# Kernel tuning notes

Hardware: AMD Instinct MI355X
Metric: run time of the kernel (lower is better)

Reference implementation:

```python
import jax, jax.numpy as jnp
import numpy as np

B, V, MAX_TOPK = 256, 128000, 256
IGNORED = -3000.0

def setup_inputs() -> dict:
    key = jax.random.key(0)
    k1, k2, k3, k4, k5 = jax.random.split(key, 5)
    token_logits = jax.random.normal(k1, (B, V), dtype=jnp.float32)
    # sampling_params[:,0]=top_k in [1,256], [:,1]=top_p in [0.5,1.0], [:,2]=temperature in [0.7,1.3]
    top_k = jax.random.randint(k2, (B,), 1, MAX_TOPK + 1).astype(jnp.float32)
    top_p = jax.random.uniform(k3, (B,), minval=0.5, maxval=1.0, dtype=jnp.float32)
    temp = jax.random.uniform(k4, (B,), minval=0.7, maxval=1.3, dtype=jnp.float32)
    sampling_params = jnp.stack([top_k, top_p, temp], axis=1)
    rand_u = jax.random.uniform(k5, (B, 1), dtype=jnp.float32)
    return {"token_logits": token_logits, "sampling_params": sampling_params, "rand_u": rand_u}

def reference(token_logits, sampling_params, rand_u):
    top_k = sampling_params[:, 0:1]        # [B,1] float
    top_p = sampling_params[:, 1:2]        # [B,1]
    temperature = sampling_params[:, 2:3]  # [B,1]
    # top_k candidates over full vocab (max_topk optimization path)
    vals, idx = jax.lax.top_k(token_logits, MAX_TOPK)  # [B,K], [B,K]
    # per-row top_k mask: positions >= top_k get IGNORED
    pos = jnp.arange(MAX_TOPK, dtype=jnp.float32)[None, :]
    vals = jnp.where(pos >= top_k, IGNORED, vals)
    # temperature
    vals = vals / temperature
    probs = jax.nn.softmax(vals, axis=-1)
    csum = jnp.cumsum(probs, axis=-1)
    # top_p clamped by global min of cumsum (matches torch.max(torch.min(csum), top_p))
    top_p_eff = jnp.maximum(jnp.min(csum), top_p)
    pmask = (csum > top_p_eff).at[:, 0].set(False)
    vals = jnp.where(pmask, IGNORED, vals)
    probs = jax.nn.softmax(vals, axis=-1)
    # multinomial via cumsum + rand-compare-sum
    csum2 = jnp.cumsum(probs, axis=-1)
    counts = jnp.sum((rand_u > csum2).astype(jnp.int32), axis=-1)  # [B]
    tokens = jnp.take_along_axis(idx, counts[:, None], axis=-1).reshape(-1)  # [B]
    return tokens
```

## Files before the change

### kernel.cpp

```cpp
#include <hip/hip_runtime.h>
#include <hip/hip_bf16.h>

constexpr int BATCH = 256;
constexpr int VOCAB = 128000;
constexpr int K = 256;
constexpr float IGNORED_C = -3000.0f;

constexpr int NCHUNK = 8;
constexpr int CHUNK = VOCAB / NCHUNK;
constexpr int N4 = CHUNK / 4;
constexpr int BINS = 8192;
constexpr int SHIFT = 19;
constexpr int CAP = 512;

constexpr int FB_BINS = 8192;
constexpr int FB_SHIFT = 19;
constexpr int FB_CAND = 2048;

__device__ __forceinline__ unsigned mono(unsigned u) {
    return (u & 0x80000000u) ? ~u : (u | 0x80000000u);
}
__device__ __forceinline__ float inv_mono(unsigned k) {
    unsigned u = (k & 0x80000000u) ? (k ^ 0x80000000u) : ~k;
    return __uint_as_float(u);
}

__global__ __launch_bounds__(512)
void k1_topk_chunk(const float* __restrict__ logits,
                   unsigned long long* __restrict__ ws_cand)
{
    __shared__ unsigned hist[BINS];
    __shared__ unsigned part[512];
    __shared__ unsigned long long cand[CAP];
    __shared__ unsigned ccount;
    __shared__ int s_tbin;

    const int tid = threadIdx.x;
    const int row = blockIdx.x >> 3;
    const int chunk = blockIdx.x & 7;
    const int gbase = chunk * CHUNK;
    const float4* rp4 = reinterpret_cast<const float4*>(
        logits + (size_t)row * VOCAB + (size_t)gbase);

    for (int i = tid; i < BINS; i += 512) hist[i] = 0u;
    if (tid == 0) ccount = 0u;
    __syncthreads();

    for (int i = tid; i < N4; i += 1024) {
        const float4 va = rp4[i];
        const bool hb = (i + 512) < N4;
        float4 vb;
        if (hb) vb = rp4[i + 512];
        atomicAdd(&hist[mono(__float_as_uint(va.x)) >> SHIFT], 1u);
        atomicAdd(&hist[mono(__float_as_uint(va.y)) >> SHIFT], 1u);
        atomicAdd(&hist[mono(__float_as_uint(va.z)) >> SHIFT], 1u);
        atomicAdd(&hist[mono(__float_as_uint(va.w)) >> SHIFT], 1u);
        if (hb) {
            atomicAdd(&hist[mono(__float_as_uint(vb.x)) >> SHIFT], 1u);
            atomicAdd(&hist[mono(__float_as_uint(vb.y)) >> SHIFT], 1u);
            atomicAdd(&hist[mono(__float_as_uint(vb.z)) >> SHIFT], 1u);
            atomicAdd(&hist[mono(__float_as_uint(vb.w)) >> SHIFT], 1u);
        }
    }
    __syncthreads();

    {
        unsigned s = 0;
        #pragma unroll
        for (int j = 0; j < 16; ++j)
            s += hist[tid * 16 + ((j + tid) & 15)];
        part[tid] = s;
    }
    __syncthreads();

    if (tid < 64) {
        const int l = tid;
        const unsigned g0 = part[l * 8 + 0], g1 = part[l * 8 + 1];
        const unsigned g2 = part[l * 8 + 2], g3 = part[l * 8 + 3];
        const unsigned g4 = part[l * 8 + 4], g5 = part[l * 8 + 5];
        const unsigned g6 = part[l * 8 + 6], g7 = part[l * 8 + 7];
        const unsigned s7 = g7;
        const unsigned s6 = s7 + g6;
        const unsigned s5 = s6 + g5;
        const unsigned s4 = s5 + g4;
        const unsigned s3 = s4 + g3;
        const unsigned s2 = s3 + g2;
        const unsigned s1 = s2 + g1;
        const unsigned s0 = s1 + g0;
        unsigned suf = s0;
        #pragma unroll
        for (int off = 1; off < 64; off <<= 1) {
            unsigned t = __shfl_down(suf, off);
            if (l + off < 64) suf += t;
        }
        const unsigned hi = suf - s0;
        const bool finder = (hi < (unsigned)K) && (hi + s0 >= (unsigned)K);
        int jj; unsigned base;
        if      (hi + s7 >= (unsigned)K) { jj = 7; base = hi; }
        else if (hi + s6 >= (unsigned)K) { jj = 6; base = hi + s7; }
        else if (hi + s5 >= (unsigned)K) { jj = 5; base = hi + s6; }
        else if (hi + s4 >= (unsigned)K) { jj = 4; base = hi + s5; }
        else if (hi + s3 >= (unsigned)K) { jj = 3; base = hi + s4; }
        else if (hi + s2 >= (unsigned)K) { jj = 2; base = hi + s3; }
        else if (hi + s1 >= (unsigned)K) { jj = 1; base = hi + s2; }
        else                             { jj = 0; base = hi + s1; }
        int tg = l * 8 + jj;
        const unsigned long long fm = __ballot(finder);
        const int src = __ffsll((unsigned long long)fm) - 1;
        tg   = __shfl(tg, src);
        base = __shfl(base, src);
        unsigned h = (l < 16) ? hist[tg * 16 + l] : 0u;
        unsigned suf16 = h;
        #pragma unroll
        for (int off = 1; off < 16; off <<= 1) {
            unsigned t = __shfl_down(suf16, off);
            if (l + off < 16) suf16 += t;
        }
        const bool qual = (l < 16) && (base + suf16 >= (unsigned)K);
        const unsigned long long qm = __ballot(qual);
        if (l == 0) s_tbin = tg * 16 + (63 - __builtin_clzll(qm));
    }
    __syncthreads();

    const unsigned tb = (unsigned)s_tbin;
#define COLV(vv, off4) { \
    const unsigned k_ = mono(__float_as_uint(vv)); \
    if ((k_ >> SHIFT) >= tb) { \
        const unsigned p_ = atomicAdd(&ccount, 1u); \
        if (p_ < (unsigned)CAP) \
            cand[p_] = ((unsigned long long)k_ << 32) | (unsigned)(~(off4)); \
    } }
    for (int i = tid; i < N4; i += 1024) {
        const float4 va = rp4[i];
        const bool hb = (i + 512) < N4;
        float4 vb;
        if (hb) vb = rp4[i + 512];
        const int ba = gbase + i * 4;
        COLV(va.x, ba + 0) COLV(va.y, ba + 1) COLV(va.z, ba + 2) COLV(va.w, ba + 3)
        if (hb) {
            const int bb = gbase + (i + 512) * 4;
            COLV(vb.x, bb + 0) COLV(vb.y, bb + 1) COLV(vb.z, bb + 2) COLV(vb.w, bb + 3)
        }
    }
#undef COLV
    __syncthreads();
    const unsigned cc = ccount;
    if ((unsigned)tid >= cc) cand[tid] = 0ull;
    __syncthreads();

    unsigned long long v = cand[tid];
    #pragma unroll
    for (int kk = 2; kk <= CAP; kk <<= 1) {
        for (int j = kk >> 1; j > 0; j >>= 1) {
            const bool keepMax = (((tid & kk) == 0) == ((tid & j) == 0));
            unsigned long long w;
            if (j >= 64) {
                __syncthreads();
                cand[tid] = v;
                __syncthreads();
                w = cand[tid ^ j];
            } else {
                w = __shfl_xor(v, j);
            }
            v = keepMax ? (v >= w ? v : w) : (v <= w ? v : w);
        }
    }

    if (tid < K) ws_cand[(size_t)blockIdx.x * K + tid] = v;
}

__global__ __launch_bounds__(1024)
void k2_merge(const float* __restrict__ params,
              const unsigned long long* __restrict__ ws_cand,
              float* __restrict__ ws_v, float* __restrict__ ws_csum,
              int* __restrict__ ws_idx, float* __restrict__ ws_p0)
{
    constexpr int N = NCHUNK * K;
    __shared__ unsigned long long cand[N];
    __shared__ float red[K];
    __shared__ float sc[K];

    const int row = blockIdx.x;
    const int tid = threadIdx.x;

    for (int i = tid; i < N; i += 1024) {
        const int c = i >> 8, pos = i & (K - 1);
        unsigned long long v = ws_cand[(size_t)row * N + i];
        const int dest = (c & 1) ? ((c << 8) | (K - 1 - pos)) : i;
        cand[dest] = v;
    }
    __syncthreads();

    for (int kk2 = 2 * K; kk2 <= N; kk2 <<= 1) {
        for (int j = kk2 >> 1; j > 0; j >>= 1) {
            for (int i = tid; i < N; i += 1024) {
                const int ixj = i ^ j;
                if (ixj > i) {
                    unsigned long long a = cand[i], b = cand[ixj];
                    bool sw = ((i & kk2) == 0) ? (a < b) : (a > b);
                    if (sw) { cand[i] = b; cand[ixj] = a; }
                }
            }
            __syncthreads();
        }
    }

    const bool act = tid < K;
    const float topk_f = params[row * 3 + 0];
    const float temp   = params[row * 3 + 2];
    float v = 0.f;
    int myidx = 0;
    if (act) {
        unsigned long long c = cand[tid];
        float val = inv_mono((unsigned)(c >> 32));
        myidx = (int)(~(unsigned)c);
        float x = (((float)tid) >= topk_f) ? IGNORED_C : val;
        v = x / temp;
        red[tid] = v;
    }
    __syncthreads();
    for (int s = K / 2; s > 0; s >>= 1) {
        if (tid < s) red[tid] = fmaxf(red[tid], red[tid + s]);
        __syncthreads();
    }
    const float m = red[0];
    __syncthreads();
    const float e = act ? expf(v - m) : 0.f;
    if (act) red[tid] = e;
    __syncthreads();
    for (int s = K / 2; s > 0; s >>= 1) {
        if (tid < s) red[tid] += red[tid + s];
        __syncthreads();
    }
    const float ssum = red[0];
    __syncthreads();
    const float p = e / ssum;
    if (act) sc[tid] = p;
    __syncthreads();
    for (int off = 1; off < K; off <<= 1) {
        float t = 0.f;
        if (act && tid >= off) t = sc[tid - off];
        __syncthreads();
        if (act) sc[tid] += t;
        __syncthreads();
    }
    if (act) {
        ws_v[row * K + tid]    = v;
        ws_csum[row * K + tid] = sc[tid];
        ws_idx[row * K + tid]  = myidx;
    }
    if (tid == 0) ws_p0[row] = p;
}

__global__ __launch_bounds__(K)
void k3_sample(const float* __restrict__ params,
               const float* __restrict__ rand_u,
               const float* __restrict__ ws_v,
               const float* __restrict__ ws_csum,
               const int* __restrict__ ws_idx,
               const float* __restrict__ ws_p0,
               int* __restrict__ out)
{
    __shared__ float red[K];
    __shared__ float sc[K];
    const int row = blockIdx.x;
    const int tid = threadIdx.x;

    red[tid] = ws_p0[tid];
    __syncthreads();
    for (int s = K / 2; s > 0; s >>= 1) {
        if (tid < s) red[tid] = fminf(red[tid], red[tid + s]);
        __syncthreads();
    }
    const float tpe = fmaxf(red[0], params[row * 3 + 1]);
    __syncthreads();

    const float csum = ws_csum[row * K + tid];
    const float v0   = ws_v[row * K + tid];
    const float v2 = ((csum > tpe) && (tid != 0)) ? IGNORED_C : v0;
    red[tid] = v2;
    __syncthreads();
    for (int s = K / 2; s > 0; s >>= 1) {
        if (tid < s) red[tid] = fmaxf(red[tid], red[tid + s]);
        __syncthreads();
    }
    const float m = red[0];
    __syncthreads();
    const float e = expf(v2 - m);
    red[tid] = e;
    __syncthreads();
    for (int s = K / 2; s > 0; s >>= 1) {
        if (tid < s) red[tid] += red[tid + s];
        __syncthreads();
    }
    const float ssum = red[0];
    __syncthreads();
    const float p = e / ssum;
    sc[tid] = p;
    __syncthreads();
    for (int off = 1; off < K; off <<= 1) {
        float t = (tid >= off) ? sc[tid - off] : 0.f;
        __syncthreads();
        sc[tid] += t;
        __syncthreads();
    }
    const float ru = rand_u[row];
    red[tid] = (ru > sc[tid]) ? 1.f : 0.f;
    __syncthreads();
    for (int s = K / 2; s > 0; s >>= 1) {
        if (tid < s) red[tid] += red[tid + s];
        __syncthreads();
    }
    if (tid == 0) {
        int sel = (int)red[0];
        if (sel > K - 1) sel = K - 1;
        out[row] = ws_idx[row * K + sel];
    }
}

__global__ __launch_bounds__(1024)
void fb_stage1(const float* __restrict__ logits,
               const float* __restrict__ params,
               float* __restrict__ ws_v,
               float* __restrict__ ws_csum,
               int* __restrict__ ws_idx,
               float* __restrict__ ws_p0)
{
    __shared__ unsigned hist[FB_BINS];
    __shared__ unsigned gsum[128];
    __shared__ unsigned long long cand[FB_CAND];
    __shared__ unsigned ccount;
    __shared__ int tbin;
    __shared__ float sv[K];
    __shared__ float se[K];
    __shared__ int   sidx[K];
    __shared__ float sred;

    const int row = blockIdx.x;
    const int tid = threadIdx.x;
    const float4* rp4 = reinterpret_cast<const float4*>(logits + (size_t)row * VOCAB);

    for (int i = tid; i < FB_BINS; i += 1024) hist[i] = 0u;
    __syncthreads();
    for (int i = tid; i < VOCAB / 4; i += 1024) {
        float4 v = rp4[i];
        atomicAdd(&hist[mono(__float_as_uint(v.x)) >> FB_SHIFT], 1u);
        atomicAdd(&hist[mono(__float_as_uint(v.y)) >> FB_SHIFT], 1u);
        atomicAdd(&hist[mono(__float_as_uint(v.z)) >> FB_SHIFT], 1u);
        atomicAdd(&hist[mono(__float_as_uint(v.w)) >> FB_SHIFT], 1u);
    }
    __syncthreads();
    if (tid < 128) {
        unsigned s = 0;
        for (int i = 0; i < 64; ++i) s += hist[tid * 64 + i];
        gsum[tid] = s;
    }
    __syncthreads();
    if (tid == 0) {
        unsigned acc = 0;
        int g = 127;
        for (; g > 0; --g) {
            if (acc + gsum[g] >= (unsigned)K) break;
            acc += gsum[g];
        }
        int t = g * 64;
        for (int bin = g * 64 + 63; bin >= g * 64; --bin) {
            acc += hist[bin];
            if (acc >= (unsigned)K) { t = bin; break; }
        }
        tbin = t;
        ccount = 0u;
    }
    __syncthreads();
    const unsigned tb = (unsigned)tbin;
    for (int i = tid; i < VOCAB / 4; i += 1024) {
        float4 v = rp4[i];
        const int base = i * 4;
        unsigned kk[4] = { mono(__float_as_uint(v.x)), mono(__float_as_uint(v.y)),
                           mono(__float_as_uint(v.z)), mono(__float_as_uint(v.w)) };
        #pragma unroll
        for (int c = 0; c < 4; ++c) {
            if ((kk[c] >> FB_SHIFT) >= tb) {
                unsigned p = atomicAdd(&ccount, 1u);
                if (p < FB_CAND)
                    cand[p] = ((unsigned long long)kk[c] << 32) | (unsigned)(~(base + c));
            }
        }
    }
    __syncthreads();
    for (int i = tid; i < FB_CAND; i += 1024)
        if ((unsigned)i >= ccount) cand[i] = 0ull;
    __syncthreads();
    for (int k = 2; k <= FB_CAND; k <<= 1) {
        for (int j = k >> 1; j > 0; j >>= 1) {
            for (int i = tid; i < FB_CAND; i += 1024) {
                int ixj = i ^ j;
                if (ixj > i) {
                    unsigned long long a = cand[i], b = cand[ixj];
                    bool sw = ((i & k) == 0) ? (a < b) : (a > b);
                    if (sw) { cand[i] = b; cand[ixj] = a; }
                }
            }
            __syncthreads();
        }
    }
    const float topk_f = params[row * 3 + 0];
    const float temp   = params[row * 3 + 2];
    if (tid < K) {
        unsigned long long c = cand[tid];
        float val = inv_mono((unsigned)(c >> 32));
        sidx[tid] = (int)(~(unsigned)c);
        float v = (((float)tid) >= topk_f) ? IGNORED_C : val;
        sv[tid] = v / temp;
    }
    __syncthreads();
    if (tid == 0) {
        float mm = sv[0];
        for (int i = 1; i < K; ++i) mm = fmaxf(mm, sv[i]);
        sred = mm;
    }
    __syncthreads();
    if (tid < K) se[tid] = expf(sv[tid] - sred);
    __syncthreads();
    if (tid == 0) {
        float s = 0.f;
        for (int i = 0; i < K; ++i) s += se[i];
        sred = s;
    }
    __syncthreads();
    if (tid < K) se[tid] = se[tid] / sred;
    __syncthreads();
    if (tid == 0) {
        float c = 0.f;
        for (int i = 0; i < K; ++i) { c += se[i]; se[i] = c; }
    }
    __syncthreads();
    if (tid < K) {
        ws_v[row * K + tid]    = sv[tid];
        ws_csum[row * K + tid] = se[tid];
        ws_idx[row * K + tid]  = sidx[tid];
    }
    if (tid == 0) ws_p0[row] = se[0];
}

extern "C" void kernel_launch(void* const* d_in, const int* in_sizes, int n_in,
                              void* d_out, int out_size, void* d_ws, size_t ws_size,
                              hipStream_t stream) {
    const float* logits = (const float*)d_in[0];
    const float* params = (const float*)d_in[1];
    const float* randu  = (const float*)d_in[2];
    int* out = (int*)d_out;
    char* ws = (char*)d_ws;

    const size_t cand_bytes = (size_t)BATCH * NCHUNK * K * 8;
    const size_t tail_bytes = (size_t)3 * BATCH * K * 4 + BATCH * 4;
    if (ws_size >= cand_bytes + tail_bytes) {
        unsigned long long* ws_cand = (unsigned long long*)ws;
        char* p = ws + cand_bytes;
        float* ws_v    = (float*)(p);
        float* ws_csum = (float*)(p + (size_t)BATCH * K * 4);
        int*   ws_idx  = (int*)  (p + (size_t)2 * BATCH * K * 4);
        float* ws_p0   = (float*)(p + (size_t)3 * BATCH * K * 4);
        hipLaunchKernelGGL(k1_topk_chunk, dim3(BATCH * NCHUNK), dim3(512), 0, stream,
                           logits, ws_cand);
        hipLaunchKernelGGL(k2_merge, dim3(BATCH), dim3(1024), 0, stream,
                           params, ws_cand, ws_v, ws_csum, ws_idx, ws_p0);
        hipLaunchKernelGGL(k3_sample, dim3(BATCH), dim3(K), 0, stream,
                           params, randu, ws_v, ws_csum, ws_idx, ws_p0, out);
    } else {
        float* ws_v    = (float*)(ws);
        float* ws_csum = (float*)(ws + (size_t)BATCH * K * 4);
        int*   ws_idx  = (int*)  (ws + (size_t)2 * BATCH * K * 4);
        float* ws_p0   = (float*)(ws + (size_t)3 * BATCH * K * 4);
        hipLaunchKernelGGL(fb_stage1, dim3(BATCH), dim3(1024), 0, stream,
                           logits, params, ws_v, ws_csum, ws_idx, ws_p0);
        hipLaunchKernelGGL(k3_sample, dim3(BATCH), dim3(K), 0, stream,
                           params, randu, ws_v, ws_csum, ws_idx, ws_p0, out);
    }
}
```

Measured before the change: 78.97 us.

## Estimate per-chunk top-k threshold from a sample histogram with exact fallback

Builds the per-chunk histogram from a 2000-element sample using packed 16-bit bins instead of the full 16000-element chunk, picking a threshold bin so that about 46 sampled values sit above it. This aims to cut the histogram pass's reads and LDS atomics. If the collected candidate count is outside [K, CAP], an exact fallback binary-searches the key threshold (and index ties) with repeated counting passes. The candidate buffer grows to 1024 entries and is sorted with a shared-memory bitonic sort, so every stage needs a block-wide barrier. That adds sort cost, and rows where the sample misleads take the slow fallback path.

```diff
diff --git a/kernel.cpp b/kernel.cpp
--- a/kernel.cpp
+++ b/kernel.cpp
@@ -11,7 +11,8 @@
 constexpr int N4 = CHUNK / 4;
 constexpr int BINS = 8192;
 constexpr int SHIFT = 19;
-constexpr int CAP = 512;
+constexpr int CAP = 1024;
+constexpr unsigned SGOAL = 46;
 
 constexpr int FB_BINS = 8192;
 constexpr int FB_SHIFT = 19;
@@ -29,46 +30,43 @@
 void k1_topk_chunk(const float* __restrict__ logits,
                    unsigned long long* __restrict__ ws_cand)
 {
-    __shared__ unsigned hist[BINS];
+    __shared__ unsigned hist[BINS / 2];
     __shared__ unsigned part[512];
     __shared__ unsigned long long cand[CAP];
+    __shared__ unsigned wred[16];
     __shared__ unsigned ccount;
     __shared__ int s_tbin;
 
     const int tid = threadIdx.x;
+    const int wave = tid >> 6, lane = tid & 63;
     const int row = blockIdx.x >> 3;
     const int chunk = blockIdx.x & 7;
     const int gbase = chunk * CHUNK;
     const float4* rp4 = reinterpret_cast<const float4*>(
         logits + (size_t)row * VOCAB + (size_t)gbase);
 
-    for (int i = tid; i < BINS; i += 512) hist[i] = 0u;
+    for (int i = tid; i < BINS / 2; i += 512) hist[i] = 0u;
     if (tid == 0) ccount = 0u;
     __syncthreads();
 
-    for (int i = tid; i < N4; i += 1024) {
-        const float4 va = rp4[i];
-        const bool hb = (i + 512) < N4;
-        float4 vb;
-        if (hb) vb = rp4[i + 512];
-        atomicAdd(&hist[mono(__float_as_uint(va.x)) >> SHIFT], 1u);
-        atomicAdd(&hist[mono(__float_as_uint(va.y)) >> SHIFT], 1u);
-        atomicAdd(&hist[mono(__float_as_uint(va.z)) >> SHIFT], 1u);
-        atomicAdd(&hist[mono(__float_as_uint(va.w)) >> SHIFT], 1u);
-        if (hb) {
-            atomicAdd(&hist[mono(__float_as_uint(vb.x)) >> SHIFT], 1u);
-            atomicAdd(&hist[mono(__float_as_uint(vb.y)) >> SHIFT], 1u);
-            atomicAdd(&hist[mono(__float_as_uint(vb.z)) >> SHIFT], 1u);
-            atomicAdd(&hist[mono(__float_as_uint(vb.w)) >> SHIFT], 1u);
-        }
+    if (tid < 500) {
+        const int seg = tid / 125, off = tid % 125;
+        const float4 v = rp4[seg * 1000 + off];
+        unsigned b;
+        b = mono(__float_as_uint(v.x)) >> SHIFT; atomicAdd(&hist[b >> 1], 1u << ((b & 1) * 16));
+        b = mono(__float_as_uint(v.y)) >> SHIFT; atomicAdd(&hist[b >> 1], 1u << ((b & 1) * 16));
+        b = mono(__float_as_uint(v.z)) >> SHIFT; atomicAdd(&hist[b >> 1], 1u << ((b & 1) * 16));
+        b = mono(__float_as_uint(v.w)) >> SHIFT; atomicAdd(&hist[b >> 1], 1u << ((b & 1) * 16));
     }
     __syncthreads();
 
     {
         unsigned s = 0;
         #pragma unroll
-        for (int j = 0; j < 16; ++j)
-            s += hist[tid * 16 + ((j + tid) & 15)];
+        for (int j = 0; j < 8; ++j) {
+            const unsigned w = hist[tid * 8 + ((j + tid) & 7)];
+            s += (w & 0xFFFFu) + (w >> 16);
+        }
         part[tid] = s;
     }
     __syncthreads();
@@ -94,29 +92,33 @@
             if (l + off < 64) suf += t;
         }
         const unsigned hi = suf - s0;
-        const bool finder = (hi < (unsigned)K) && (hi + s0 >= (unsigned)K);
+        const bool finder = (hi < SGOAL) && (hi + s0 >= SGOAL);
         int jj; unsigned base;
-        if      (hi + s7 >= (unsigned)K) { jj = 7; base = hi; }
-        else if (hi + s6 >= (unsigned)K) { jj = 6; base = hi + s7; }
-        else if (hi + s5 >= (unsigned)K) { jj = 5; base = hi + s6; }
-        else if (hi + s4 >= (unsigned)K) { jj = 4; base = hi + s5; }
-        else if (hi + s3 >= (unsigned)K) { jj = 3; base = hi + s4; }
-        else if (hi + s2 >= (unsigned)K) { jj = 2; base = hi + s3; }
-        else if (hi + s1 >= (unsigned)K) { jj = 1; base = hi + s2; }
-        else                             { jj = 0; base = hi + s1; }
+        if      (hi + s7 >= SGOAL) { jj = 7; base = hi; }
+        else if (hi + s6 >= SGOAL) { jj = 6; base = hi + s7; }
+        else if (hi + s5 >= SGOAL) { jj = 5; base = hi + s6; }
+        else if (hi + s4 >= SGOAL) { jj = 4; base = hi + s5; }
+        else if (hi + s3 >= SGOAL) { jj = 3; base = hi + s4; }
+        else if (hi + s2 >= SGOAL) { jj = 2; base = hi + s3; }
+        else if (hi + s1 >= SGOAL) { jj = 1; base = hi + s2; }
+        else                       { jj = 0; base = hi + s1; }
         int tg = l * 8 + jj;
         const unsigned long long fm = __ballot(finder);
         const int src = __ffsll((unsigned long long)fm) - 1;
         tg   = __shfl(tg, src);
         base = __shfl(base, src);
-        unsigned h = (l < 16) ? hist[tg * 16 + l] : 0u;
+        unsigned h = 0u;
+        if (l < 16) {
+            const unsigned w = hist[tg * 8 + (l >> 1)];
+            h = (w >> ((l & 1) * 16)) & 0xFFFFu;
+        }
         unsigned suf16 = h;
         #pragma unroll
         for (int off = 1; off < 16; off <<= 1) {
             unsigned t = __shfl_down(suf16, off);
             if (l + off < 16) suf16 += t;
         }
-        const bool qual = (l < 16) && (base + suf16 >= (unsigned)K);
+        const bool qual = (l < 16) && (base + suf16 >= SGOAL);
         const unsigned long long qm = __ballot(qual);
         if (l == 0) s_tbin = tg * 16 + (63 - __builtin_clzll(qm));
     }
@@ -144,29 +146,103 @@
     }
 #undef COLV
     __syncthreads();
-    const unsigned cc = ccount;
-    if ((unsigned)tid >= cc) cand[tid] = 0ull;
-    __syncthreads();
-
-    unsigned long long v = cand[tid];
-    #pragma unroll
-    for (int kk = 2; kk <= CAP; kk <<= 1) {
-        for (int j = kk >> 1; j > 0; j >>= 1) {
-            const bool keepMax = (((tid & kk) == 0) == ((tid & j) == 0));
-            unsigned long long w;
-            if (j >= 64) {
-                __syncthreads();
-                cand[tid] = v;
-                __syncthreads();
-                w = cand[tid ^ j];
-            } else {
-                w = __shfl_xor(v, j);
+    unsigned cc = ccount;
+    __syncthreads();
+
+#define COUNT_KEY(Tv, Xv, NGT, NEQ) do { \
+    const unsigned T_ = (Tv), X_ = (Xv); \
+    unsigned cgt = 0u, ceq = 0u; \
+    for (int i_ = tid; i_ < N4; i_ += 512) { \
+        const float4 v_ = rp4[i_]; \
+        const unsigned b_ = 4u * (unsigned)i_; \
+        unsigned kk_; \
+        kk_ = mono(__float_as_uint(v_.x)); cgt += (kk_ > T_); ceq += ((kk_ == T_) && (b_ + 0u <= X_)); \
+        kk_ = mono(__float_as_uint(v_.y)); cgt += (kk_ > T_); ceq += ((kk_ == T_) && (b_ + 1u <= X_)); \
+        kk_ = mono(__float_as_uint(v_.z)); cgt += (kk_ > T_); ceq += ((kk_ == T_) && (b_ + 2u <= X_)); \
+        kk_ = mono(__float_as_uint(v_.w)); cgt += (kk_ > T_); ceq += ((kk_ == T_) && (b_ + 3u <= X_)); \
+    } \
+    for (int o_ = 32; o_ >= 1; o_ >>= 1) { cgt += __shfl_xor(cgt, o_); ceq += __shfl_xor(ceq, o_); } \
+    __syncthreads(); \
+    if (lane == 0) { wred[wave] = cgt; wred[8 + wave] = ceq; } \
+    __syncthreads(); \
+    unsigned g_ = 0u, e_ = 0u; \
+    for (int w_ = 0; w_ < 8; ++w_) { g_ += wred[w_]; e_ += wred[8 + w_]; } \
+    (NGT) = g_; (NEQ) = e_; \
+} while (0)
+
+    if (cc < (unsigned)K || cc > (unsigned)CAP) {
+        unsigned g, e, T;
+        bool tie = false; unsigned X = 0xFFFFFFFFu;
+        COUNT_KEY(0xFFFFFFFFu, 0xFFFFFFFFu, g, e);
+        if (g + e >= (unsigned)K) {
+            T = 0xFFFFFFFFu;
+        } else {
+            unsigned klo = 0u, khi = 0xFFFFFFFFu;
+            while (khi - klo > 1u) {
+                const unsigned mid = klo + ((khi - klo) >> 1);
+                COUNT_KEY(mid, 0xFFFFFFFFu, g, e);
+                if (g + e >= (unsigned)K) klo = mid; else khi = mid;
             }
-            v = keepMax ? (v >= w ? v : w) : (v <= w ? v : w);
-        }
-    }
-
-    if (tid < K) ws_cand[(size_t)blockIdx.x * K + tid] = v;
+            T = klo;
+        }
+        COUNT_KEY(T, 0xFFFFFFFFu, g, e);
+        if (g + e > (unsigned)CAP) {
+            tie = true;
+            const unsigned target = (unsigned)K - g;
+            int xlo = -1, xhi = CHUNK - 1;
+            while (xhi - xlo > 1) {
+                const int xm = (xlo + xhi) >> 1;
+                unsigned g2, e2;
+                COUNT_KEY(T, (unsigned)xm, g2, e2);
+                if (e2 >= target) xhi = xm; else xlo = xm;
+            }
+            X = (unsigned)xhi;
+        }
+        if (tid == 0) ccount = 0u;
+        __syncthreads();
+        for (int i = tid; i < N4; i += 512) {
+            const float4 v = rp4[i];
+            const unsigned b = 4u * (unsigned)i;
+#define FCOL(kx, off) { \
+        const unsigned kk_ = (kx); \
+        if ((kk_ > T) || ((kk_ == T) && (!tie || (b + (off)) <= X))) { \
+            const unsigned p_ = atomicAdd(&ccount, 1u); \
+            if (p_ < (unsigned)CAP) \
+                cand[p_] = ((unsigned long long)kk_ << 32) \
+                         | (unsigned)(~(unsigned)(gbase + (int)(b + (off)))); \
+        } }
+            FCOL(mono(__float_as_uint(v.x)), 0u)
+            FCOL(mono(__float_as_uint(v.y)), 1u)
+            FCOL(mono(__float_as_uint(v.z)), 2u)
+            FCOL(mono(__float_as_uint(v.w)), 3u)
+#undef FCOL
+        }
+        __syncthreads();
+        cc = ccount;
+        __syncthreads();
+    }
+#undef COUNT_KEY
+
+    const unsigned stored = (cc < (unsigned)CAP) ? cc : (unsigned)CAP;
+    for (int i = tid; i < CAP; i += 512)
+        if ((unsigned)i >= stored) cand[i] = 0ull;
+    __syncthreads();
+
+    for (int k = 2; k <= CAP; k <<= 1) {
+        for (int j = k >> 1; j > 0; j >>= 1) {
+            for (int i = tid; i < CAP; i += 512) {
+                const int ixj = i ^ j;
+                if (ixj > i) {
+                    const unsigned long long a = cand[i], b = cand[ixj];
+                    const bool sw = ((i & k) == 0) ? (a < b) : (a > b);
+                    if (sw) { cand[i] = b; cand[ixj] = a; }
+                }
+            }
+            __syncthreads();
+        }
+    }
+
+    if (tid < K) ws_cand[(size_t)blockIdx.x * K + tid] = cand[tid];
 }
 
 __global__ __launch_bounds__(1024)
```

Measured after the change: 103.8 us. 1.31x slower.
